# Performance work log

Measured on AMD Instinct MI355X. Metric: run time of the kernel, lower is better.

The kernel has to match this reference:

```python
import jax, jax.numpy as jnp
import numpy as np

KS = 3          # deformable kernel size
N = KS * KS     # 9 sampling points
PAD = 1         # zero padding before sampling


def setup_inputs() -> dict:
    key = jax.random.key(0)
    k = jax.random.split(key, 4)
    b, c, h, w = 8, 64, 128, 128
    x = jax.random.normal(k[0], (b, c, h, w), jnp.float32)
    # offset-prediction conv: Conv2d(c, 2*N, 3, padding=1, stride=1) with bias
    w_off = jax.random.normal(k[1], (2 * N, c, 3, 3), jnp.float32) * 0.01
    b_off = jax.random.normal(k[2], (2 * N,), jnp.float32) * 0.01
    # main conv: Conv2d(c, c, 3, stride=3, bias=None) applied to rearranged samples
    w_conv = jax.random.normal(k[3], (c, c, KS, KS), jnp.float32) * (1.0 / np.sqrt(c * N))
    return {"x": x, "w_off": w_off, "b_off": b_off, "w_conv": w_conv}


def _deform_conv2d(x, w_off, b_off, w_conv):
    b, c, h, w = x.shape
    # 1) predict offsets: (b, 2N, h, w)
    offset = jax.lax.conv_general_dilated(
        x, w_off, (1, 1), ((PAD, PAD), (PAD, PAD)),
        dimension_numbers=("NCHW", "OIHW", "NCHW"))
    offset = offset + b_off[None, :, None, None]
    offset = offset.transpose(0, 2, 3, 1)  # (b, h, w, 2N), first N = rows, last N = cols

    # 2) sampling positions p = p_0 + p_n + offset (in zero-padded coords)
    dx, dy = jnp.meshgrid(
        jnp.arange(-(KS - 1) // 2, (KS - 1) // 2 + 1),
        jnp.arange(-(KS - 1) // 2, (KS - 1) // 2 + 1), indexing="ij")
    pn_x = dx.reshape(-1).astype(x.dtype)  # (N,)
    pn_y = dy.reshape(-1).astype(x.dtype)
    r0 = jnp.arange(1, h + 1, dtype=x.dtype)  # p_0 starts at 1 (padding shift)
    c0 = jnp.arange(1, w + 1, dtype=x.dtype)
    p_x = offset[..., :N] + pn_x + r0[None, :, None, None]   # (b,h,w,N)
    p_y = offset[..., N:] + pn_y + c0[None, None, :, None]

    xp = jnp.pad(x, ((0, 0), (0, 0), (PAD, PAD), (PAD, PAD)))
    Hp, Wp = h + 2 * PAD, w + 2 * PAD

    fx = jnp.floor(p_x)
    fy = jnp.floor(p_y)
    q_lt_x = jnp.clip(fx, 0, Hp - 1).astype(jnp.int32)
    q_lt_y = jnp.clip(fy, 0, Wp - 1).astype(jnp.int32)
    q_rb_x = jnp.clip(fx + 1, 0, Hp - 1).astype(jnp.int32)
    q_rb_y = jnp.clip(fy + 1, 0, Wp - 1).astype(jnp.int32)
    p_x = jnp.clip(p_x, 0, Hp - 1)
    p_y = jnp.clip(p_y, 0, Wp - 1)

    # bilinear weights (b,h,w,N); q values are non-differentiable (int)
    g_lt = (1 + (q_lt_x - p_x)) * (1 + (q_lt_y - p_y))
    g_rb = (1 - (q_rb_x - p_x)) * (1 - (q_rb_y - p_y))
    g_lb = (1 + (q_lt_x - p_x)) * (1 - (q_rb_y - p_y))
    g_rt = (1 - (q_rb_x - p_x)) * (1 + (q_lt_y - p_y))

    xp_flat = xp.reshape(b, c, Hp * Wp)

    def gather(qx, qy):
        idx = (qx * Wp + qy).reshape(b, 1, h * w * N)
        out = jnp.take_along_axis(
            xp_flat, jnp.broadcast_to(idx, (b, c, h * w * N)), axis=2)
        return out.reshape(b, c, h, w, N)

    x_off = (g_lt[:, None] * gather(q_lt_x, q_lt_y)
             + g_rb[:, None] * gather(q_rb_x, q_rb_y)
             + g_lb[:, None] * gather(q_lt_x, q_rb_y)
             + g_rt[:, None] * gather(q_rb_x, q_lt_y))  # (b,c,h,w,N)

    # 3) final KSxKS conv with stride KS over the rearranged samples is exactly
    #    a contraction over the N sampling points (sample n = kernel tap (i,j), n=i*KS+j)
    out = jnp.einsum("bchwn,ocn->bohw", x_off, w_conv.reshape(c, c, N))
    return out


def reference(x, w_off, b_off, w_conv):
    return _deform_conv2d(x, w_off, b_off, w_conv) + x
```

## Files before the change

kernel.cpp:

```cpp
#include <hip/hip_runtime.h>


typedef short bf16x8 __attribute__((ext_vector_type(8)));
typedef float f32x4  __attribute__((ext_vector_type(4)));

#define MFMA16(a, b, c) __builtin_amdgcn_mfma_f32_16x16x32_bf16(a, b, c, 0, 0, 0)
#define GTAG 0x40000000
#define OFFS 21

__device__ __forceinline__ float bflo(unsigned w) { return __builtin_bit_cast(float, w << 16); }
__device__ __forceinline__ float bfhi(unsigned w) { return __builtin_bit_cast(float, w & 0xffff0000u); }
__device__ __forceinline__ unsigned short f2bf(float f) {
    unsigned u = __builtin_bit_cast(unsigned, f);
    u += 0x7fffu + ((u >> 16) & 1u);
    return (unsigned short)(u >> 16);
}
__device__ __forceinline__ unsigned packbf(float lo, float hi) {
    return __builtin_amdgcn_perm(__builtin_bit_cast(unsigned, hi),
                                 __builtin_bit_cast(unsigned, lo), 0x07060302u);
}

__global__ __launch_bounds__(256) void k_prep_xt(const float* __restrict__ x,
                                                 unsigned short* __restrict__ xt) {
    __shared__ float xs[64][129];
    const int bh = blockIdx.x;
    const int h = bh & 127, b = bh >> 7;
    const float* xr = x + ((size_t)b * 64 * 128 + h) * 128;
    for (int idx = threadIdx.x; idx < 8192; idx += 256) {
        int c = idx >> 7, w = idx & 127;
        xs[c][w] = xr[(size_t)c * 16384 + w];
    }
    __syncthreads();
    unsigned short* xto = xt + ((size_t)bh << 13);
    for (int j = threadIdx.x; j < 1024; j += 256) {
        int w = j >> 3, c0 = (j & 7) << 3;
        unsigned short tmp[8];
#pragma unroll
        for (int e = 0; e < 8; ++e) tmp[e] = f2bf(xs[c0 + e][w]);
        *(uint4*)(xto + w * 64 + c0) = *(const uint4*)tmp;
    }
}

__global__ void k_prep_w(const float* __restrict__ w_conv, const float* __restrict__ w_off,
                         unsigned short* __restrict__ w_m2, unsigned short* __restrict__ woff2) {
    int t = blockIdx.x * 256 + threadIdx.x;
    if (t < 36864) {
        int r = t & 511;
        int fid = t >> 9;
        int l15 = r >> 5, q4 = (r >> 3) & 3, e = t & 7;
        int chunk = fid & 1, of = (fid >> 1) & 3, n = fid >> 3;
        int o = of * 16 + l15, c = chunk * 32 + q4 * 8 + e;
        w_m2[t] = f2bf(w_conv[(o * 64 + c) * 9 + n]);
    }
    int t2 = t - 36864;
    if (t2 >= 0 && t2 < 18432) {
        int r = t2 & 511;
        int fid = t2 >> 9;
        int l15 = r >> 5, q4 = (r >> 3) & 3, e = t2 & 7;
        int kc = fid & 1, half = (fid >> 1) & 1, rj = fid >> 2;
        int k = half * 16 + l15, c = kc * 32 + q4 * 8 + e;
        woff2[t2] = (k < 18) ? f2bf(w_off[(k * 64 + c) * 9 + rj]) : (unsigned short)0;
    }
}

__global__ __launch_bounds__(256, 2) void k_fused(
    const float* __restrict__ x, const unsigned short* __restrict__ xt,
    const unsigned short* __restrict__ w_m2, const unsigned short* __restrict__ woff2,
    const float* __restrict__ b_off, float* __restrict__ out) {

    __shared__ __align__(16) unsigned char raw[420 * 128];
    __shared__ int   atab[9][64][4];
    __shared__ float gtab[9][64][4];
    __shared__ float offv[64 * OFFS];
    __shared__ int   sfb;

    const int wk = ((blockIdx.x & 7) << 8) + (blockIdx.x >> 3);
    const int b = wk >> 8, h = (wk >> 1) & 127, wt = (wk & 1) << 6;

    const int tid  = threadIdx.x;
    const int lane = tid & 63, wid = tid >> 6;
    const int l15  = lane & 15, q4 = lane >> 4;
    const int lofs = ((l15 << 2) + q4) << 3;
    const int px   = wid * 16 + l15;

    const unsigned short* xtb = xt + ((size_t)b << 20);

    if (tid == 0) sfb = 0;

    for (int idx = tid; idx < 3360; idx += 256) {
        int rec = idx >> 3, cc = idx & 7;
        int row = rec / 70, col = rec - row * 70;
        int xr = h - 2 + row, xc = wt - 3 + col;
        uint4 v = make_uint4(0, 0, 0, 0);
        if (xr >= 0 && xr < 128 && xc >= 0 && xc < 128)
            v = *(const uint4*)(xtb + ((((size_t)xr << 7) + xc) << 6) + (cc << 3));
        *(uint4*)(raw + (rec << 7) + ((cc ^ (col & 7)) << 4)) = v;
    }
    __syncthreads();

    {
        f32x4 o0 = {0.f, 0.f, 0.f, 0.f}, o1 = {0.f, 0.f, 0.f, 0.f};
#pragma unroll
        for (int rj = 0; rj < 9; ++rj) {
            const int dr = rj / 3, dj = rj % 3;
            const int colw = px + dj + 2;
            const int recb = (dr + 1) * 70 + colw;
            const int swz  = colw & 7;
#pragma unroll
            for (int kc = 0; kc < 2; ++kc) {
                bf16x8 bfrag = *(const bf16x8*)(raw + (recb << 7) + ((((kc << 2) + q4) ^ swz) << 4));
                bf16x8 a0 = *(const bf16x8*)(woff2 + ((((rj * 2 + 0) << 1) + kc) << 9) + lofs);
                bf16x8 a1 = *(const bf16x8*)(woff2 + ((((rj * 2 + 1) << 1) + kc) << 9) + lofs);
                o0 = MFMA16(a0, bfrag, o0);
                o1 = MFMA16(a1, bfrag, o1);
            }
        }
#pragma unroll
        for (int rg = 0; rg < 4; ++rg) {
            int o = q4 * 4 + rg;
            offv[px * OFFS + o] = o0[rg] + b_off[o];
            int o1i = 16 + o;
            if (o1i < 18) offv[px * OFFS + o1i] = o1[rg] + b_off[o1i];
        }
    }
    __syncthreads();

    for (int idx = tid; idx < 576; idx += 256) {
        const int n = idx >> 6, p = idx & 63;
        float ox = offv[p * OFFS + n], oy = offv[p * OFFS + 9 + n];
        float pxf = ox + (float)(n / 3 - 1) + (float)(h + 1);
        float pyf = oy + (float)(n % 3 - 1) + (float)(wt + p + 1);
        float fx = floorf(pxf), fy = floorf(pyf);
        float fxc  = fminf(fmaxf(fx, 0.f), 129.f);
        float fyc  = fminf(fmaxf(fy, 0.f), 129.f);
        float fxc1 = fminf(fmaxf(fx + 1.f, 0.f), 129.f);
        float fyc1 = fminf(fmaxf(fy + 1.f, 0.f), 129.f);
        int qltx = (int)fxc, qlty = (int)fyc, qrbx = (int)fxc1, qrby = (int)fyc1;
        pxf = fminf(fmaxf(pxf, 0.f), 129.f);
        pyf = fminf(fmaxf(pyf, 0.f), 129.f);
        float glt = (1.f + (fxc  - pxf)) * (1.f + (fyc  - pyf));
        float grb = (1.f - (fxc1 - pxf)) * (1.f - (fyc1 - pyf));
        float glb = (1.f + (fxc  - pxf)) * (1.f - (fyc1 - pyf));
        float grt = (1.f - (fxc1 - pxf)) * (1.f + (fyc  - pyf));
        bool vlx = (qltx >= 1) & (qltx <= 128), vly = (qlty >= 1) & (qlty <= 128);
        bool vrx = (qrbx >= 1) & (qrbx <= 128), vry = (qrby >= 1) & (qrby <= 128);

        auto enc = [&](int qx, int qy, bool val) -> int {
            if (!val) return 0;
            int wr = qx - h + 1;
            int wc = qy - wt + 2;
            if (wr >= 0 && wr < 6 && wc >= 0 && wc < 70)
                return ((wr * 70 + wc) << 7) | ((wc & 7) << 4);
            return GTAG | ((((qx - 1) << 7) + (qy - 1)) << 6);
        };
        int a0 = enc(qltx, qlty, vlx & vly);
        int a1 = enc(qrbx, qrby, vrx & vry);
        int a2 = enc(qltx, qrby, vlx & vry);
        int a3 = enc(qrbx, qlty, vrx & vly);
        if ((a0 | a1 | a2 | a3) & GTAG) sfb = 1;
        if (!(vlx & vly)) glt = 0.f;
        if (!(vrx & vry)) grb = 0.f;
        if (!(vlx & vry)) glb = 0.f;
        if (!(vrx & vly)) grt = 0.f;
        *(int4*)&atab[n][p][0]   = make_int4(a0, a1, a2, a3);
        *(float4*)&gtab[n][p][0] = make_float4(glt, grb, glb, grt);
    }
    __syncthreads();

    const size_t obase = ((size_t)b * 64 * 128 + h) * 128 + wt + px;
    float xres[4][4];
#pragma unroll
    for (int of = 0; of < 4; ++of)
#pragma unroll
        for (int rg = 0; rg < 4; ++rg)
            xres[of][rg] = x[obase + (size_t)(of * 16 + q4 * 4 + rg) * 16384];

    f32x4 acc[4];
#pragma unroll
    for (int of = 0; of < 4; ++of) acc[of] = (f32x4){0.f, 0.f, 0.f, 0.f};

    if (!sfb) {
#pragma unroll
        for (int n = 0; n < 9; ++n) {
            const int4   av = *(const int4*)&atab[n][px][0];
            const float4 gv = *(const float4*)&gtab[n][px][0];
            const int ee[4] = {av.x, av.y, av.z, av.w};
            uint4 clo[4], chi[4];
#pragma unroll
            for (int j = 0; j < 4; ++j) {
                const unsigned char* lp = raw + (ee[j] & ~127);
                int sl = ((q4 ^ (ee[j] >> 4)) & 7) << 4;
                clo[j] = *(const uint4*)(lp + sl);
                chi[j] = *(const uint4*)(lp + (sl ^ 64));
            }
            unsigned owl[4], owh[4];
            {
                const unsigned* p0 = (const unsigned*)&clo[0];
                const unsigned* p1 = (const unsigned*)&clo[1];
                const unsigned* p2 = (const unsigned*)&clo[2];
                const unsigned* p3 = (const unsigned*)&clo[3];
                const unsigned* h0 = (const unsigned*)&chi[0];
                const unsigned* h1 = (const unsigned*)&chi[1];
                const unsigned* h2 = (const unsigned*)&chi[2];
                const unsigned* h3 = (const unsigned*)&chi[3];
#pragma unroll
                for (int d = 0; d < 4; ++d) {
                    float flo = fmaf(gv.x, bflo(p0[d]), fmaf(gv.y, bflo(p1[d]), fmaf(gv.z, bflo(p2[d]), gv.w * bflo(p3[d]))));
                    float fhi = fmaf(gv.x, bfhi(p0[d]), fmaf(gv.y, bfhi(p1[d]), fmaf(gv.z, bfhi(p2[d]), gv.w * bfhi(p3[d]))));
                    owl[d] = packbf(flo, fhi);
                    float glo = fmaf(gv.x, bflo(h0[d]), fmaf(gv.y, bflo(h1[d]), fmaf(gv.z, bflo(h2[d]), gv.w * bflo(h3[d]))));
                    float ghi = fmaf(gv.x, bfhi(h0[d]), fmaf(gv.y, bfhi(h1[d]), fmaf(gv.z, bfhi(h2[d]), gv.w * bfhi(h3[d]))));
                    owh[d] = packbf(glo, ghi);
                }
            }
            bf16x8 bfr0 = *(const bf16x8*)&owl[0];
            bf16x8 bfr1 = *(const bf16x8*)&owh[0];
            const unsigned short* wn = w_m2 + (n << 12);
#pragma unroll
            for (int of = 0; of < 4; ++of) {
                bf16x8 a0 = *(const bf16x8*)(wn + (((of << 1) + 0) << 9) + lofs);
                bf16x8 a1 = *(const bf16x8*)(wn + (((of << 1) + 1) << 9) + lofs);
                acc[of] = MFMA16(a0, bfr0, acc[of]);
                acc[of] = MFMA16(a1, bfr1, acc[of]);
            }
        }
    } else {
        for (int n = 0; n < 9; ++n) {
            const int4   av = *(const int4*)&atab[n][px][0];
            const float4 gv = *(const float4*)&gtab[n][px][0];
            const int ee[4] = {av.x, av.y, av.z, av.w};
            uint4 clo[4], chi[4];
#pragma unroll
            for (int j = 0; j < 4; ++j) {
                int e = ee[j];
                if (e & GTAG) {
                    const unsigned short* gp = xtb + (e & (GTAG - 1));
                    clo[j] = *(const uint4*)(gp + (q4 << 3));
                    chi[j] = *(const uint4*)(gp + (q4 << 3) + 32);
                } else {
                    const unsigned char* lp = raw + (e & ~127);
                    int sl = ((q4 ^ (e >> 4)) & 7) << 4;
                    clo[j] = *(const uint4*)(lp + sl);
                    chi[j] = *(const uint4*)(lp + (sl ^ 64));
                }
            }
            unsigned owl[4], owh[4];
            {
                const unsigned* p0 = (const unsigned*)&clo[0];
                const unsigned* p1 = (const unsigned*)&clo[1];
                const unsigned* p2 = (const unsigned*)&clo[2];
                const unsigned* p3 = (const unsigned*)&clo[3];
                const unsigned* h0 = (const unsigned*)&chi[0];
                const unsigned* h1 = (const unsigned*)&chi[1];
                const unsigned* h2 = (const unsigned*)&chi[2];
                const unsigned* h3 = (const unsigned*)&chi[3];
#pragma unroll
                for (int d = 0; d < 4; ++d) {
                    float flo = fmaf(gv.x, bflo(p0[d]), fmaf(gv.y, bflo(p1[d]), fmaf(gv.z, bflo(p2[d]), gv.w * bflo(p3[d]))));
                    float fhi = fmaf(gv.x, bfhi(p0[d]), fmaf(gv.y, bfhi(p1[d]), fmaf(gv.z, bfhi(p2[d]), gv.w * bfhi(p3[d]))));
                    owl[d] = packbf(flo, fhi);
                    float glo = fmaf(gv.x, bflo(h0[d]), fmaf(gv.y, bflo(h1[d]), fmaf(gv.z, bflo(h2[d]), gv.w * bflo(h3[d]))));
                    float ghi = fmaf(gv.x, bfhi(h0[d]), fmaf(gv.y, bfhi(h1[d]), fmaf(gv.z, bfhi(h2[d]), gv.w * bfhi(h3[d]))));
                    owh[d] = packbf(glo, ghi);
                }
            }
            bf16x8 bfr0 = *(const bf16x8*)&owl[0];
            bf16x8 bfr1 = *(const bf16x8*)&owh[0];
            const unsigned short* wn = w_m2 + (n << 12);
#pragma unroll
            for (int of = 0; of < 4; ++of) {
                bf16x8 a0 = *(const bf16x8*)(wn + (((of << 1) + 0) << 9) + lofs);
                bf16x8 a1 = *(const bf16x8*)(wn + (((of << 1) + 1) << 9) + lofs);
                acc[of] = MFMA16(a0, bfr0, acc[of]);
                acc[of] = MFMA16(a1, bfr1, acc[of]);
            }
        }
    }

#pragma unroll
    for (int of = 0; of < 4; ++of)
#pragma unroll
        for (int rg = 0; rg < 4; ++rg)
            out[obase + (size_t)(of * 16 + q4 * 4 + rg) * 16384] = acc[of][rg] + xres[of][rg];
}

extern "C" void kernel_launch(void* const* d_in, const int* in_sizes, int n_in,
                              void* d_out, int out_size, void* d_ws, size_t ws_size,
                              hipStream_t stream) {
    const float* x      = (const float*)d_in[0];
    const float* w_off  = (const float*)d_in[1];
    const float* b_off  = (const float*)d_in[2];
    const float* w_conv = (const float*)d_in[3];

    unsigned short* xt    = (unsigned short*)d_ws;
    unsigned short* w_m2  = xt + (size_t)8 * 128 * 128 * 64;
    unsigned short* woff2 = w_m2 + 9 * 64 * 64;

    hipLaunchKernelGGL(k_prep_xt, dim3(1024), dim3(256), 0, stream, x, xt);
    hipLaunchKernelGGL(k_prep_w,  dim3(216),  dim3(256), 0, stream, w_conv, w_off, w_m2, woff2);
    hipLaunchKernelGGL(k_fused,   dim3(2048), dim3(256), 0, stream,
                       x, xt, w_m2, woff2, b_off, (float*)d_out);
}
```

Before: 97.42 us.

## Switch bf16 pipeline to fp16 with packed half2 bilinear blending and weight prefetch

Converts the staged input, offset weights and conv weights from bf16 to fp16 and uses f16 MFMA instructions. The bilinear blend now runs in packed half2 FMAs using pre-packed fp16 gate weights, replacing the fp32 unpack/fma/repack sequence. Conv weights for the next sampling point are also prefetched into registers (double buffered) in the fast path. This cuts VALU work in the gather-blend stage but raises register pressure and accumulates the blend in fp16, which reduces precision.

Result: faster. 93.24 us (-4.3%).

```diff
diff --git a/kernel.cpp b/kernel.cpp
--- a/kernel.cpp
+++ b/kernel.cpp
@@ -1,23 +1,18 @@
 #include <hip/hip_runtime.h>
 
 
-typedef short bf16x8 __attribute__((ext_vector_type(8)));
-typedef float f32x4  __attribute__((ext_vector_type(4)));
-
-#define MFMA16(a, b, c) __builtin_amdgcn_mfma_f32_16x16x32_bf16(a, b, c, 0, 0, 0)
+typedef _Float16 h2    __attribute__((ext_vector_type(2)));
+typedef _Float16 f16x8 __attribute__((ext_vector_type(8)));
+typedef float    f32x4 __attribute__((ext_vector_type(4)));
+
+#define MFMAH(a, b, c) __builtin_amdgcn_mfma_f32_16x16x32_f16(a, b, c, 0, 0, 0)
 #define GTAG 0x40000000
 #define OFFS 21
 
-__device__ __forceinline__ float bflo(unsigned w) { return __builtin_bit_cast(float, w << 16); }
-__device__ __forceinline__ float bfhi(unsigned w) { return __builtin_bit_cast(float, w & 0xffff0000u); }
-__device__ __forceinline__ unsigned short f2bf(float f) {
-    unsigned u = __builtin_bit_cast(unsigned, f);
-    u += 0x7fffu + ((u >> 16) & 1u);
-    return (unsigned short)(u >> 16);
-}
-__device__ __forceinline__ unsigned packbf(float lo, float hi) {
-    return __builtin_amdgcn_perm(__builtin_bit_cast(unsigned, hi),
-                                 __builtin_bit_cast(unsigned, lo), 0x07060302u);
+__device__ __forceinline__ h2 bch2(unsigned u) { return __builtin_bit_cast(h2, u); }
+__device__ __forceinline__ unsigned bcu(h2 v) { return __builtin_bit_cast(unsigned, v); }
+__device__ __forceinline__ unsigned short f2h(float f) {
+    return __builtin_bit_cast(unsigned short, (_Float16)f);
 }
 
 __global__ __launch_bounds__(256) void k_prep_xt(const float* __restrict__ x,
@@ -36,7 +31,7 @@
         int w = j >> 3, c0 = (j & 7) << 3;
         unsigned short tmp[8];
 #pragma unroll
-        for (int e = 0; e < 8; ++e) tmp[e] = f2bf(xs[c0 + e][w]);
+        for (int e = 0; e < 8; ++e) tmp[e] = f2h(xs[c0 + e][w]);
         *(uint4*)(xto + w * 64 + c0) = *(const uint4*)tmp;
     }
 }
@@ -50,7 +45,7 @@
         int l15 = r >> 5, q4 = (r >> 3) & 3, e = t & 7;
         int chunk = fid & 1, of = (fid >> 1) & 3, n = fid >> 3;
         int o = of * 16 + l15, c = chunk * 32 + q4 * 8 + e;
-        w_m2[t] = f2bf(w_conv[(o * 64 + c) * 9 + n]);
+        w_m2[t] = f2h(w_conv[(o * 64 + c) * 9 + n]);
     }
     int t2 = t - 36864;
     if (t2 >= 0 && t2 < 18432) {
@@ -59,7 +54,7 @@
         int l15 = r >> 5, q4 = (r >> 3) & 3, e = t2 & 7;
         int kc = fid & 1, half = (fid >> 1) & 1, rj = fid >> 2;
         int k = half * 16 + l15, c = kc * 32 + q4 * 8 + e;
-        woff2[t2] = (k < 18) ? f2bf(w_off[(k * 64 + c) * 9 + rj]) : (unsigned short)0;
+        woff2[t2] = (k < 18) ? f2h(w_off[(k * 64 + c) * 9 + rj]) : (unsigned short)0;
     }
 }
 
@@ -70,7 +65,7 @@
 
     __shared__ __align__(16) unsigned char raw[420 * 128];
     __shared__ int   atab[9][64][4];
-    __shared__ float gtab[9][64][4];
+    __shared__ uint4 gtab[9][64];
     __shared__ float offv[64 * OFFS];
     __shared__ int   sfb;
 
@@ -108,11 +103,11 @@
             const int swz  = colw & 7;
 #pragma unroll
             for (int kc = 0; kc < 2; ++kc) {
-                bf16x8 bfrag = *(const bf16x8*)(raw + (recb << 7) + ((((kc << 2) + q4) ^ swz) << 4));
-                bf16x8 a0 = *(const bf16x8*)(woff2 + ((((rj * 2 + 0) << 1) + kc) << 9) + lofs);
-                bf16x8 a1 = *(const bf16x8*)(woff2 + ((((rj * 2 + 1) << 1) + kc) << 9) + lofs);
-                o0 = MFMA16(a0, bfrag, o0);
-                o1 = MFMA16(a1, bfrag, o1);
+                f16x8 bfrag = *(const f16x8*)(raw + (recb << 7) + ((((kc << 2) + q4) ^ swz) << 4));
+                f16x8 a0 = *(const f16x8*)((const _Float16*)woff2 + ((((rj * 2 + 0) << 1) + kc) << 9) + lofs);
+                f16x8 a1 = *(const f16x8*)((const _Float16*)woff2 + ((((rj * 2 + 1) << 1) + kc) << 9) + lofs);
+                o0 = MFMAH(a0, bfrag, o0);
+                o1 = MFMAH(a1, bfrag, o1);
             }
         }
 #pragma unroll
@@ -162,8 +157,13 @@
         if (!(vrx & vry)) grb = 0.f;
         if (!(vlx & vry)) glb = 0.f;
         if (!(vrx & vly)) grt = 0.f;
-        *(int4*)&atab[n][p][0]   = make_int4(a0, a1, a2, a3);
-        *(float4*)&gtab[n][p][0] = make_float4(glt, grb, glb, grt);
+        auto pk = [](float g) -> unsigned {
+            _Float16 t = (_Float16)g;
+            h2 r = {t, t};
+            return __builtin_bit_cast(unsigned, r);
+        };
+        *(int4*)&atab[n][p][0] = make_int4(a0, a1, a2, a3);
+        gtab[n][p] = make_uint4(pk(glt), pk(grb), pk(glb), pk(grt));
     }
     __syncthreads();
 
@@ -179,11 +179,55 @@
 #pragma unroll
     for (int of = 0; of < 4; ++of) acc[of] = (f32x4){0.f, 0.f, 0.f, 0.f};
 
+    const _Float16* wmh = (const _Float16*)w_m2;
+    f16x8 wreg[2][2][4];
+#pragma unroll
+    for (int of = 0; of < 4; ++of) {
+        wreg[0][0][of] = *(const f16x8*)(wmh + (((of << 1) + 0) << 9) + lofs);
+        wreg[0][1][of] = *(const f16x8*)(wmh + (((of << 1) + 1) << 9) + lofs);
+    }
+
+    auto blend = [&](const uint4* clo, const uint4* chi, uint4 gq, f16x8& bfr0, f16x8& bfr1) {
+        h2 g0 = bch2(gq.x), g1 = bch2(gq.y), g2 = bch2(gq.z), g3 = bch2(gq.w);
+        const unsigned* c0 = (const unsigned*)&clo[0];
+        const unsigned* c1 = (const unsigned*)&clo[1];
+        const unsigned* c2 = (const unsigned*)&clo[2];
+        const unsigned* c3 = (const unsigned*)&clo[3];
+        const unsigned* e0 = (const unsigned*)&chi[0];
+        const unsigned* e1 = (const unsigned*)&chi[1];
+        const unsigned* e2 = (const unsigned*)&chi[2];
+        const unsigned* e3 = (const unsigned*)&chi[3];
+        unsigned owl[4], owh[4];
+#pragma unroll
+        for (int d = 0; d < 4; ++d) {
+            h2 sl = bch2(c0[d]) * g0;
+            sl = __builtin_elementwise_fma(bch2(c1[d]), g1, sl);
+            sl = __builtin_elementwise_fma(bch2(c2[d]), g2, sl);
+            sl = __builtin_elementwise_fma(bch2(c3[d]), g3, sl);
+            owl[d] = bcu(sl);
+            h2 sh = bch2(e0[d]) * g0;
+            sh = __builtin_elementwise_fma(bch2(e1[d]), g1, sh);
+            sh = __builtin_elementwise_fma(bch2(e2[d]), g2, sh);
+            sh = __builtin_elementwise_fma(bch2(e3[d]), g3, sh);
+            owh[d] = bcu(sh);
+        }
+        bfr0 = __builtin_bit_cast(f16x8, *(const uint4*)owl);
+        bfr1 = __builtin_bit_cast(f16x8, *(const uint4*)owh);
+    };
+
     if (!sfb) {
 #pragma unroll
         for (int n = 0; n < 9; ++n) {
-            const int4   av = *(const int4*)&atab[n][px][0];
-            const float4 gv = *(const float4*)&gtab[n][px][0];
+            if (n < 8) {
+                const _Float16* wn1 = wmh + ((n + 1) << 12);
+#pragma unroll
+                for (int of = 0; of < 4; ++of) {
+                    wreg[(n + 1) & 1][0][of] = *(const f16x8*)(wn1 + (((of << 1) + 0) << 9) + lofs);
+                    wreg[(n + 1) & 1][1][of] = *(const f16x8*)(wn1 + (((of << 1) + 1) << 9) + lofs);
+                }
+            }
+            const int4  av = *(const int4*)&atab[n][px][0];
+            const uint4 gq = gtab[n][px];
             const int ee[4] = {av.x, av.y, av.z, av.w};
             uint4 clo[4], chi[4];
 #pragma unroll
@@ -193,41 +237,18 @@
                 clo[j] = *(const uint4*)(lp + sl);
                 chi[j] = *(const uint4*)(lp + (sl ^ 64));
             }
-            unsigned owl[4], owh[4];
-            {
-                const unsigned* p0 = (const unsigned*)&clo[0];
-                const unsigned* p1 = (const unsigned*)&clo[1];
-                const unsigned* p2 = (const unsigned*)&clo[2];
-                const unsigned* p3 = (const unsigned*)&clo[3];
-                const unsigned* h0 = (const unsigned*)&chi[0];
-                const unsigned* h1 = (const unsigned*)&chi[1];
-                const unsigned* h2 = (const unsigned*)&chi[2];
-                const unsigned* h3 = (const unsigned*)&chi[3];
-#pragma unroll
-                for (int d = 0; d < 4; ++d) {
-                    float flo = fmaf(gv.x, bflo(p0[d]), fmaf(gv.y, bflo(p1[d]), fmaf(gv.z, bflo(p2[d]), gv.w * bflo(p3[d]))));
-                    float fhi = fmaf(gv.x, bfhi(p0[d]), fmaf(gv.y, bfhi(p1[d]), fmaf(gv.z, bfhi(p2[d]), gv.w * bfhi(p3[d]))));
-                    owl[d] = packbf(flo, fhi);
-                    float glo = fmaf(gv.x, bflo(h0[d]), fmaf(gv.y, bflo(h1[d]), fmaf(gv.z, bflo(h2[d]), gv.w * bflo(h3[d]))));
-                    float ghi = fmaf(gv.x, bfhi(h0[d]), fmaf(gv.y, bfhi(h1[d]), fmaf(gv.z, bfhi(h2[d]), gv.w * bfhi(h3[d]))));
-                    owh[d] = packbf(glo, ghi);
-                }
-            }
-            bf16x8 bfr0 = *(const bf16x8*)&owl[0];
-            bf16x8 bfr1 = *(const bf16x8*)&owh[0];
-            const unsigned short* wn = w_m2 + (n << 12);
+            f16x8 bfr0, bfr1;
+            blend(clo, chi, gq, bfr0, bfr1);
 #pragma unroll
             for (int of = 0; of < 4; ++of) {
-                bf16x8 a0 = *(const bf16x8*)(wn + (((of << 1) + 0) << 9) + lofs);
-                bf16x8 a1 = *(const bf16x8*)(wn + (((of << 1) + 1) << 9) + lofs);
-                acc[of] = MFMA16(a0, bfr0, acc[of]);
-                acc[of] = MFMA16(a1, bfr1, acc[of]);
+                acc[of] = MFMAH(wreg[n & 1][0][of], bfr0, acc[of]);
+                acc[of] = MFMAH(wreg[n & 1][1][of], bfr1, acc[of]);
             }
         }
     } else {
         for (int n = 0; n < 9; ++n) {
-            const int4   av = *(const int4*)&atab[n][px][0];
-            const float4 gv = *(const float4*)&gtab[n][px][0];
+            const int4  av = *(const int4*)&atab[n][px][0];
+            const uint4 gq = gtab[n][px];
             const int ee[4] = {av.x, av.y, av.z, av.w};
             uint4 clo[4], chi[4];
 #pragma unroll
@@ -244,35 +265,15 @@
                     chi[j] = *(const uint4*)(lp + (sl ^ 64));
                 }
             }
-            unsigned owl[4], owh[4];
-            {
-                const unsigned* p0 = (const unsigned*)&clo[0];
-                const unsigned* p1 = (const unsigned*)&clo[1];
-                const unsigned* p2 = (const unsigned*)&clo[2];
-                const unsigned* p3 = (const unsigned*)&clo[3];
-                const unsigned* h0 = (const unsigned*)&chi[0];
-                const unsigned* h1 = (const unsigned*)&chi[1];
-                const unsigned* h2 = (const unsigned*)&chi[2];
-                const unsigned* h3 = (const unsigned*)&chi[3];
-#pragma unroll
-                for (int d = 0; d < 4; ++d) {
-                    float flo = fmaf(gv.x, bflo(p0[d]), fmaf(gv.y, bflo(p1[d]), fmaf(gv.z, bflo(p2[d]), gv.w * bflo(p3[d]))));
-                    float fhi = fmaf(gv.x, bfhi(p0[d]), fmaf(gv.y, bfhi(p1[d]), fmaf(gv.z, bfhi(p2[d]), gv.w * bfhi(p3[d]))));
-                    owl[d] = packbf(flo, fhi);
-                    float glo = fmaf(gv.x, bflo(h0[d]), fmaf(gv.y, bflo(h1[d]), fmaf(gv.z, bflo(h2[d]), gv.w * bflo(h3[d]))));
-                    float ghi = fmaf(gv.x, bfhi(h0[d]), fmaf(gv.y, bfhi(h1[d]), fmaf(gv.z, bfhi(h2[d]), gv.w * bfhi(h3[d]))));
-                    owh[d] = packbf(glo, ghi);
-                }
-            }
-            bf16x8 bfr0 = *(const bf16x8*)&owl[0];
-            bf16x8 bfr1 = *(const bf16x8*)&owh[0];
-            const unsigned short* wn = w_m2 + (n << 12);
+            f16x8 bfr0, bfr1;
+            blend(clo, chi, gq, bfr0, bfr1);
+            const _Float16* wn = wmh + (n << 12);
 #pragma unroll
             for (int of = 0; of < 4; ++of) {
-                bf16x8 a0 = *(const bf16x8*)(wn + (((of << 1) + 0) << 9) + lofs);
-                bf16x8 a1 = *(const bf16x8*)(wn + (((of << 1) + 1) << 9) + lofs);
-                acc[of] = MFMA16(a0, bfr0, acc[of]);
-                acc[of] = MFMA16(a1, bfr1, acc[of]);
+                f16x8 a0 = *(const f16x8*)(wn + (((of << 1) + 0) << 9) + lofs);
+                f16x8 a1 = *(const f16x8*)(wn + (((of << 1) + 1) << 9) + lofs);
+                acc[of] = MFMAH(a0, bfr0, acc[of]);
+                acc[of] = MFMAH(a1, bfr1, acc[of]);
             }
         }
     }
```
